# Performance work log

Measured on AMD Instinct MI355X. Metric: run time of the kernel, lower is better.

## Reference

```python
import jax, jax.numpy as jnp
from jax import lax
import numpy as np

B, NW, L, E, H, V = 8192, 4, 16, 128, 128, 64  # batch, words/example, max chars, emsize, hidden, char vocab


def setup_inputs() -> dict:
    key = jax.random.key(0)
    ks = jax.random.split(key, 13)
    s = 0.05
    return {
        "word_ids": jax.random.randint(ks[0], (B, NW, L), 0, V, dtype=jnp.int32),
        "lengths": jax.random.randint(ks[1], (B, NW), 1, L + 1, dtype=jnp.int32),
        "emb_i": jax.random.normal(ks[2], (V, E), jnp.float32),
        "W_ih": jax.random.normal(ks[3], (4 * H, E), jnp.float32) * s,
        "W_hh": jax.random.normal(ks[4], (4 * H, H), jnp.float32) * s,
        "b_ih": jax.random.normal(ks[5], (4 * H,), jnp.float32) * s,
        "b_hh": jax.random.normal(ks[6], (4 * H,), jnp.float32) * s,
        "conv1_w": jax.random.normal(ks[7], (4, 1, 2, 2), jnp.float32) * 0.5,
        "conv1_b": jax.random.normal(ks[8], (4,), jnp.float32) * 0.1,
        "conv2_w": jax.random.normal(ks[9], (8, 4, 2, 2), jnp.float32) * 0.5,
        "conv2_b": jax.random.normal(ks[10], (8,), jnp.float32) * 0.1,
        "scorer_w": jax.random.normal(ks[11], (1, 2 * 2 * 8), jnp.float32) * 0.2,
        "scorer_b": jax.random.normal(ks[12], (1,), jnp.float32) * 0.1,
    }


def reference(word_ids, lengths, emb_i, W_ih, W_hh, b_ih, b_hh,
              conv1_w, conv1_b, conv2_w, conv2_b, scorer_w, scorer_b):
    Bx, NWx, Lx = word_ids.shape
    Hh = W_hh.shape[1]
    BN = Bx * NWx
    # char embeddings for all words, packed: [L, BN, E]
    xs = emb_i[word_ids.reshape(BN, Lx)].transpose(1, 0, 2)
    # ragged lengths -> per-step update mask [L, BN]
    mask = jnp.arange(Lx, dtype=lengths.dtype)[:, None] < lengths.reshape(-1)[None, :]
    h0 = jnp.zeros((BN, Hh), emb_i.dtype)

    def step(carry, xm):
        h, c = carry
        x_t, m = xm
        gates = x_t @ W_ih.T + b_ih + h @ W_hh.T + b_hh  # torch LSTMCell gate order i,f,g,o
        i, f, g, o = jnp.split(gates, 4, axis=-1)
        i = jax.nn.sigmoid(i); f = jax.nn.sigmoid(f)
        g = jnp.tanh(g); o = jax.nn.sigmoid(o)
        c_new = f * c + i * g
        h_new = o * jnp.tanh(c_new)
        m = m[:, None]
        return (jnp.where(m, h_new, h), jnp.where(m, c_new, c)), None

    (h, c), _ = lax.scan(step, (h0, h0), (xs, mask))
    # Model.encode returns the cell state c
    reps = c.reshape(Bx, NWx, Hh)

    # pairwise cosine similarity matrix [B, NW, NW]
    norms = jnp.sqrt(jnp.sum(reps * reps, axis=-1))
    dots = jnp.einsum('bih,bjh->bij', reps, reps)
    cos = dots / (norms[:, :, None] * norms[:, None, :])

    # tiny 2-layer CNN scorer on the NWxNW matrix (NCHW)
    dn = ('NCHW', 'OIHW', 'NCHW')
    x_img = cos[:, None, :, :]
    out = jax.nn.relu(lax.conv_general_dilated(x_img, conv1_w, (1, 1), 'VALID', dimension_numbers=dn)
                      + conv1_b[None, :, None, None])
    out = jax.nn.relu(lax.conv_general_dilated(out, conv2_w, (1, 1), 'VALID', dimension_numbers=dn)
                      + conv2_b[None, :, None, None])
    flat = out.reshape(Bx, -1)  # channel-major flatten matches torch .view
    score = flat @ scorer_w.T + scorer_b
    return jax.nn.sigmoid(score)  # [B, 1] discriminator prob
```

## Files before the change

### kernel.cpp

```cpp
#include <hip/hip_runtime.h>

#define BSZ    8192
#define NWRD   4
#define SEQL   16
#define HDIM   128
#define VOCAB  64
#define NSEQ   (BSZ * NWRD)
#define WGSEQ  32
#define UPB    80
#define BINCAP (UPB * WGSEQ)
#define NUNITS (16 * UPB)

#define AS1 __attribute__((address_space(1)))
#define AS3 __attribute__((address_space(3)))

typedef float    f32x4  __attribute__((ext_vector_type(4)));
typedef float    f32x16 __attribute__((ext_vector_type(16)));
typedef __bf16   bf16x8 __attribute__((ext_vector_type(8)));
typedef _Float16 f16x8  __attribute__((ext_vector_type(8)));
typedef int      i32x4  __attribute__((ext_vector_type(4)));

union AccU { f32x16 v; f32x4 q[4]; float f[16]; };

__device__ __forceinline__ unsigned short f2bf(float f) {
    unsigned int u = __builtin_bit_cast(unsigned int, f);
    return (unsigned short)((u + 0x7fff + ((u >> 16) & 1)) >> 16);
}
__device__ __forceinline__ float sigm(float x) {
    return __builtin_amdgcn_rcpf(1.f + __builtin_amdgcn_exp2f(x * -1.44269504f));
}

__global__ void prep4(const float* __restrict__ emb, const float* __restrict__ W_ih,
                      const float* __restrict__ b_ih, const float* __restrict__ b_hh,
                      const float* __restrict__ W_hh, const int* __restrict__ lengths,
                      unsigned short* __restrict__ P2H, unsigned short* __restrict__ WA,
                      int* __restrict__ perm, int* __restrict__ gh)
{
    __shared__ int lh[16], gbase[16];
    const int blk = blockIdx.x, tid = threadIdx.x;

    if (blk < 128) {
        int idx = blk * 256 + tid;
        int v = idx >> 9, g = (idx >> 7) & 3, j = idx & 127;
        int n = g * 128 + j;
        const f32x4* er = (const f32x4*)(emb  + v * 128);
        const f32x4* wr = (const f32x4*)(W_ih + n * 128);
        f32x4 s4 = er[0] * wr[0];
#pragma unroll
        for (int e = 1; e < 32; ++e) s4 += er[e] * wr[e];
        float s = s4.x + s4.y + s4.z + s4.w + b_ih[n] + b_hh[n];
        int wv = j >> 5, jr = j & 31;
        int d = jr & 3, hl = (jr >> 2) & 1, q = jr >> 3;
        int cc = g * 16 + wv * 4 + hl * 2 + (q >> 1);
        int F  = v * 512 + ((cc ^ (v & 7)) << 3) + (q & 1) * 4 + d;
        P2H[F] = __builtin_bit_cast(unsigned short, (_Float16)s);
    } else if (blk < 384) {
        int idx = (blk - 128) * 256 + tid;
        int jj = idx & 7, lane = (idx >> 3) & 63, kc = (idx >> 9) & 7, tt = idx >> 12;
        int wv = tt >> 2, g = tt & 3;
        int n = g * 128 + wv * 32 + (lane & 31);
        int k = kc * 16 + (lane >> 5) * 8 + jj;
        WA[idx] = f2bf(W_hh[n * 128 + k]);
    } else {
        if (tid < 16) lh[tid] = 0;
        __syncthreads();
        int i = (blk - 384) * 256 + tid;
        int b = 16 - lengths[i];
        int rank = atomicAdd(&lh[b], 1);
        __syncthreads();
        if (tid < 16) gbase[tid] = atomicAdd(&gh[tid], lh[tid]);
        __syncthreads();
        perm[b * BINCAP + gbase[b] + rank] = i;
    }
}

__global__ __launch_bounds__(256, 2) void lstm4(
    const int* __restrict__ word_ids, const int* __restrict__ perm,
    const int* __restrict__ gh, const unsigned short* __restrict__ P2H,
    const unsigned short* __restrict__ WA, float* __restrict__ c_out)
{
    __shared__ __align__(16) unsigned short ptab[VOCAB * 512];
    __shared__ __align__(16) unsigned short hbuf[2][WGSEQ * 128];

    const int tid    = threadIdx.x;
    const int wv     = tid >> 6;
    const int lane   = tid & 63;
    const int lane31 = lane & 31;
    const int hl     = lane >> 5;

    const int u    = blockIdx.x;
    const int b    = u / UPB;
    const int widx = u % UPB;
    const int cnt  = gh[b];
    if (widx * WGSEQ >= cnt) return;
    const int ml   = 16 - b;

    {
        const char* src = (const char*)P2H;
        char*       dst = (char*)ptab;
#pragma unroll
        for (int r = 0; r < 16; ++r) {
            const int off = r * 4096 + wv * 1024;
            __builtin_amdgcn_global_load_lds(
                (const AS1 unsigned int*)(src + off + lane * 16),
                (AS3 unsigned int*)(dst + off), 16, 0, 0);
        }
    }

    bf16x8 afr[4][8];
#pragma unroll
    for (int g = 0; g < 4; ++g)
#pragma unroll
        for (int kc = 0; kc < 8; ++kc)
            afr[g][kc] = *(const bf16x8*)(WA + (((wv * 4 + g) * 8 + kc) * 64 + lane) * 8);

    const int slot = widx * WGSEQ + lane31;
    const int live = slot < cnt;
    const int sid  = live ? perm[b * BINCAP + slot] : 0;
    unsigned long long u0, u1;
    {
        const i32x4* wp = (const i32x4*)(word_ids + sid * SEQL);
        i32x4 a = wp[0], b4 = wp[1], c4 = wp[2], d4 = wp[3];
        unsigned lo0 = (unsigned)(a.x  | (a.y  << 8) | (a.z  << 16) | (a.w  << 24));
        unsigned hi0 = (unsigned)(b4.x | (b4.y << 8) | (b4.z << 16) | (b4.w << 24));
        unsigned lo1 = (unsigned)(c4.x | (c4.y << 8) | (c4.z << 16) | (c4.w << 24));
        unsigned hi1 = (unsigned)(d4.x | (d4.y << 8) | (d4.z << 16) | (d4.w << 24));
        u0 = ((unsigned long long)hi0 << 32) | lo0;
        u1 = ((unsigned long long)hi1 << 32) | lo1;
    }
    __syncthreads();

    f32x4 cq[4] = {{0,0,0,0},{0,0,0,0},{0,0,0,0},{0,0,0,0}};
    const int      rdo_b = lane31 * 256;
    const unsigned xv    = (unsigned)((lane31 & 7) << 4);
    const int      jbase = wv * 32 + 4 * hl;
    const int      ccb   = wv * 4 + hl * 2;

#pragma unroll 1
    for (int t = 0; t < ml; ++t) {
        const int w = (int)(u0 & 63);
        u0 = (u0 >> 8) | (u1 << 56); u1 >>= 8;

        AccU acc[4];
        {
            const char*    rowp = (const char*)ptab + (w << 10);
            const unsigned wx   = (unsigned)((w & 7) << 4);
#pragma unroll
            for (int g = 0; g < 4; ++g)
#pragma unroll
                for (int s = 0; s < 2; ++s) {
                    const unsigned off = ((unsigned)((g * 16 + ccb + s) << 4)) ^ wx;
                    f16x8 hv = *(const f16x8*)(rowp + off);
#pragma unroll
                    for (int k = 0; k < 8; ++k)
                        acc[g].f[s * 8 + k] = (float)hv[k];
                }
        }

        if (t > 0) {
            const char* hr = (const char*)hbuf[t & 1];
            bf16x8 bfv[8];
#pragma unroll
            for (int kc = 0; kc < 8; ++kc)
                bfv[kc] = *(const bf16x8*)(hr + rdo_b +
                              (((unsigned)(kc * 32 + hl * 16)) ^ xv));
#pragma unroll
            for (int kc = 0; kc < 8; ++kc) {
                const bf16x8 bb = bfv[kc];
#pragma unroll
                for (int g = 0; g < 4; ++g)
                    acc[g].v = __builtin_amdgcn_mfma_f32_32x32x16_bf16(
                        afr[g][kc], bb, acc[g].v, 0, 0, 0);
            }
        }

        const int wr = (t < ml - 1);
        char* hw = (char*)hbuf[(t + 1) & 1];
#pragma unroll
        for (int q = 0; q < 4; ++q) {
            float hv4[4];
#pragma unroll
            for (int d = 0; d < 4; ++d) {
                const int r = q * 4 + d;
                float ei = __builtin_amdgcn_exp2f(acc[0].f[r] * -1.44269504f);
                float ef = __builtin_amdgcn_exp2f(acc[1].f[r] * -1.44269504f);
                float eg = __builtin_amdgcn_exp2f(acc[2].f[r] *  2.88539008f);
                float fg  = __builtin_amdgcn_rcpf(1.f + ef);
                float igg = (eg - 1.f) *
                            __builtin_amdgcn_rcpf((1.f + ei) * (1.f + eg));
                float cn = cq[q][d] * fg + igg;
                cq[q][d] = cn;
                if (wr) {
                    float eo = __builtin_amdgcn_exp2f(acc[3].f[r] * -1.44269504f);
                    float ec = __builtin_amdgcn_exp2f(cn * 2.88539008f);
                    hv4[d] = (ec - 1.f) *
                             __builtin_amdgcn_rcpf((1.f + eo) * (1.f + ec));
                }
            }
            if (wr) {
                unsigned int plo_, phi_;
                asm("v_cvt_pk_bf16_f32 %0, %1, %2"
                    : "=v"(plo_) : "v"(hv4[0]), "v"(hv4[1]));
                asm("v_cvt_pk_bf16_f32 %0, %1, %2"
                    : "=v"(phi_) : "v"(hv4[2]), "v"(hv4[3]));
                unsigned long long pu_ =
                    ((unsigned long long)phi_ << 32) | plo_;
                *(unsigned long long*)(hw + rdo_b +
                    (((unsigned)(wv * 64 + q * 16)) ^ xv) + hl * 8) = pu_;
            }
        }
        if (wr) __syncthreads();
    }

    if (live) {
#pragma unroll
        for (int q = 0; q < 4; ++q)
            *(f32x4*)(c_out + sid * HDIM + jbase + 8 * q) = cq[q];
    }
}

__global__ __launch_bounds__(256) void epilogue(
    const float* __restrict__ c_ws,
    const float* __restrict__ conv1_w, const float* __restrict__ conv1_b,
    const float* __restrict__ conv2_w, const float* __restrict__ conv2_b,
    const float* __restrict__ scorer_w, const float* __restrict__ scorer_b,
    float* __restrict__ out)
{
    __shared__ __align__(16) float reps[8 * NWRD * HDIM];
    __shared__ float gram_s[8 * 16];

    const int tid = threadIdx.x;
    const int b0  = blockIdx.x * 8;

    for (int i = tid; i < 8 * NWRD * HDIM; i += 256)
        reps[i] = c_ws[b0 * NWRD * HDIM + i];
    __syncthreads();

    const int bt  = tid >> 5;
    const int sub = tid & 31;

    float dval = 0.f;
    if (sub < 16) {
        int i = sub >> 2, j = sub & 3;
        const f32x4* ci = (const f32x4*)(reps + (bt * 4 + i) * HDIM);
        const f32x4* cj = (const f32x4*)(reps + (bt * 4 + j) * HDIM);
        f32x4 s4 = {0.f, 0.f, 0.f, 0.f};
        for (int k = 0; k < HDIM / 4; ++k) s4 += ci[k] * cj[k];
        dval = s4.x + s4.y + s4.z + s4.w;
        gram_s[bt * 16 + sub] = dval;
    }
    __syncthreads();
    float cosv = 0.f;
    if (sub < 16) {
        int i = sub >> 2, j = sub & 3;
        float di = gram_s[bt * 16 + i * 4 + i];
        float dj = gram_s[bt * 16 + j * 4 + j];
        cosv = __fdividef(dval, sqrtf(di * dj));
    }
    __syncthreads();
    if (sub < 16) gram_s[bt * 16 + sub] = cosv;
    __syncthreads();

    if (sub == 0) {
        float img[4][4];
#pragma unroll
        for (int i = 0; i < 4; ++i)
#pragma unroll
            for (int j = 0; j < 4; ++j) img[i][j] = gram_s[bt * 16 + i * 4 + j];

        float o1[4][3][3];
#pragma unroll
        for (int ch = 0; ch < 4; ++ch) {
            float w00 = conv1_w[ch*4+0], w01 = conv1_w[ch*4+1];
            float w10 = conv1_w[ch*4+2], w11 = conv1_w[ch*4+3];
            float bb  = conv1_b[ch];
#pragma unroll
            for (int y = 0; y < 3; ++y)
#pragma unroll
                for (int x = 0; x < 3; ++x) {
                    float s = bb + w00*img[y][x]   + w01*img[y][x+1]
                                 + w10*img[y+1][x] + w11*img[y+1][x+1];
                    o1[ch][y][x] = s > 0.f ? s : 0.f;
                }
        }
        float sc = scorer_b[0];
#pragma unroll
        for (int oc = 0; oc < 8; ++oc) {
            float bb = conv2_b[oc];
#pragma unroll
            for (int y = 0; y < 2; ++y)
#pragma unroll
                for (int x = 0; x < 2; ++x) {
                    float s = bb;
#pragma unroll
                    for (int ic = 0; ic < 4; ++ic) {
                        const float* w = conv2_w + oc * 16 + ic * 4;
                        s += w[0]*o1[ic][y][x]   + w[1]*o1[ic][y][x+1]
                           + w[2]*o1[ic][y+1][x] + w[3]*o1[ic][y+1][x+1];
                    }
                    float rl = s > 0.f ? s : 0.f;
                    sc += rl * scorer_w[oc * 4 + y * 2 + x];
                }
        }
        out[blockIdx.x * 8 + bt] = sigm(sc);
    }
}

extern "C" void kernel_launch(void* const* d_in, const int* in_sizes, int n_in,
                              void* d_out, int out_size, void* d_ws, size_t ws_size,
                              hipStream_t stream)
{
    const int*   word_ids = (const int*)d_in[0];
    const int*   lengths  = (const int*)d_in[1];
    const float* emb      = (const float*)d_in[2];
    const float* W_ih     = (const float*)d_in[3];
    const float* W_hh     = (const float*)d_in[4];
    const float* b_ih     = (const float*)d_in[5];
    const float* b_hh     = (const float*)d_in[6];
    const float* conv1_w  = (const float*)d_in[7];
    const float* conv1_b  = (const float*)d_in[8];
    const float* conv2_w  = (const float*)d_in[9];
    const float* conv2_b  = (const float*)d_in[10];
    const float* scorer_w = (const float*)d_in[11];
    const float* scorer_b = (const float*)d_in[12];
    float* out = (float*)d_out;

    char* ws = (char*)d_ws;
    unsigned short* P2H  = (unsigned short*)(ws + 0);
    unsigned short* WA   = (unsigned short*)(ws + (128<<10));
    int*            perm = (int*)(ws + (256<<10));
    int*            gh   = (int*)(ws + (416<<10));
    float*          c_ws = (float*)(ws + (512<<10));

    hipMemsetAsync(gh, 0, 16 * sizeof(int), stream);
    prep4   <<<512,   256, 0, stream>>>(emb, W_ih, b_ih, b_hh, W_hh, lengths,
                                        P2H, WA, perm, gh);
    lstm4   <<<NUNITS, 256, 0, stream>>>(word_ids, perm, gh, P2H, WA, c_ws);
    epilogue<<<BSZ / 8, 256, 0, stream>>>(c_ws, conv1_w, conv1_b, conv2_w, conv2_b,
                                          scorer_w, scorer_b, out);
}
```

Baseline: 172.3 us.

## Load input projections via identity MFMA and offload exp to FMA polynomial

The precomputed input-projection table is now loaded as f16 vectors and added into the accumulators with two identity-matrix f16 MFMAs per gate, instead of per-element f16-to-f32 conversions. The table layout in the prep kernel changes to match. Two of the transcendental exp2 calls per element are replaced by a polynomial exp2 built from FMAs, and the gate math is refactored to use a single reciprocal instead of two. The aim is to move work off the transcendental and VALU conversion paths onto the matrix and FMA units. The cost is extra MFMA instructions and a polynomial with no overflow handling.

```diff
diff --git a/kernel.cpp b/kernel.cpp
--- a/kernel.cpp
+++ b/kernel.cpp
@@ -29,6 +29,18 @@
 __device__ __forceinline__ float sigm(float x) {
     return __builtin_amdgcn_rcpf(1.f + __builtin_amdgcn_exp2f(x * -1.44269504f));
 }
+__device__ __forceinline__ float pexp2(float y) {
+    float n = __builtin_rintf(y);
+    float f = y - n;
+    float p = 1.3333558e-3f;
+    p = __builtin_fmaf(p, f, 9.6181291e-3f);
+    p = __builtin_fmaf(p, f, 5.5504109e-2f);
+    p = __builtin_fmaf(p, f, 2.4022651e-1f);
+    p = __builtin_fmaf(p, f, 6.9314718e-1f);
+    p = __builtin_fmaf(p, f, 1.0f);
+    int e = (int)n;
+    return __builtin_bit_cast(float, __builtin_bit_cast(int, p) + (e << 23));
+}
 
 __global__ void prep4(const float* __restrict__ emb, const float* __restrict__ W_ih,
                       const float* __restrict__ b_ih, const float* __restrict__ b_hh,
@@ -49,10 +61,8 @@
 #pragma unroll
         for (int e = 1; e < 32; ++e) s4 += er[e] * wr[e];
         float s = s4.x + s4.y + s4.z + s4.w + b_ih[n] + b_hh[n];
-        int wv = j >> 5, jr = j & 31;
-        int d = jr & 3, hl = (jr >> 2) & 1, q = jr >> 3;
-        int cc = g * 16 + wv * 4 + hl * 2 + (q >> 1);
-        int F  = v * 512 + ((cc ^ (v & 7)) << 3) + (q & 1) * 4 + d;
+        int cj = g * 16 + (j >> 3);
+        int F  = v * 512 + ((cj ^ (v & 7)) << 3) + (j & 7);
         P2H[F] = __builtin_bit_cast(unsigned short, (_Float16)s);
     } else if (blk < 384) {
         int idx = (blk - 128) * 256 + tid;
@@ -114,6 +124,14 @@
         for (int kc = 0; kc < 8; ++kc)
             afr[g][kc] = *(const bf16x8*)(WA + (((wv * 4 + g) * 8 + kc) * 64 + lane) * 8);
 
+    f16x8 idA0, idA1;
+#pragma unroll
+    for (int jj = 0; jj < 8; ++jj) {
+        idA0[jj] = (_Float16)((lane31 == hl * 8 + jj)      ? 1.f : 0.f);
+        idA1[jj] = (_Float16)((lane31 == 16 + hl * 8 + jj) ? 1.f : 0.f);
+    }
+    const f32x16 ZED = {0,0,0,0, 0,0,0,0, 0,0,0,0, 0,0,0,0};
+
     const int slot = widx * WGSEQ + lane31;
     const int live = slot < cnt;
     const int sid  = live ? perm[b * BINCAP + slot] : 0;
@@ -134,29 +152,25 @@
     const int      rdo_b = lane31 * 256;
     const unsigned xv    = (unsigned)((lane31 & 7) << 4);
     const int      jbase = wv * 32 + 4 * hl;
-    const int      ccb   = wv * 4 + hl * 2;
 
 #pragma unroll 1
     for (int t = 0; t < ml; ++t) {
         const int w = (int)(u0 & 63);
         u0 = (u0 >> 8) | (u1 << 56); u1 >>= 8;
+        const unsigned rowb = ((unsigned)w << 10);
+        const unsigned wx   = (unsigned)((w & 7) << 4);
+
+        f16x8 pf[4][2];
+#pragma unroll
+        for (int g = 0; g < 4; ++g)
+#pragma unroll
+            for (int s = 0; s < 2; ++s) {
+                const unsigned cj =
+                    ((unsigned)((g * 16 + wv * 4 + s * 2 + hl) << 4)) ^ wx;
+                pf[g][s] = *(const f16x8*)((const char*)ptab + rowb + cj);
+            }
 
         AccU acc[4];
-        {
-            const char*    rowp = (const char*)ptab + (w << 10);
-            const unsigned wx   = (unsigned)((w & 7) << 4);
-#pragma unroll
-            for (int g = 0; g < 4; ++g)
-#pragma unroll
-                for (int s = 0; s < 2; ++s) {
-                    const unsigned off = ((unsigned)((g * 16 + ccb + s) << 4)) ^ wx;
-                    f16x8 hv = *(const f16x8*)(rowp + off);
-#pragma unroll
-                    for (int k = 0; k < 8; ++k)
-                        acc[g].f[s * 8 + k] = (float)hv[k];
-                }
-        }
-
         if (t > 0) {
             const char* hr = (const char*)hbuf[t & 1];
             bf16x8 bfv[8];
@@ -165,12 +179,23 @@
                 bfv[kc] = *(const bf16x8*)(hr + rdo_b +
                               (((unsigned)(kc * 32 + hl * 16)) ^ xv));
 #pragma unroll
-            for (int kc = 0; kc < 8; ++kc) {
-                const bf16x8 bb = bfv[kc];
-#pragma unroll
-                for (int g = 0; g < 4; ++g)
+            for (int g = 0; g < 4; ++g) {
+                acc[g].v = __builtin_amdgcn_mfma_f32_32x32x16_f16(
+                    idA0, pf[g][0], ZED, 0, 0, 0);
+                acc[g].v = __builtin_amdgcn_mfma_f32_32x32x16_f16(
+                    idA1, pf[g][1], acc[g].v, 0, 0, 0);
+#pragma unroll
+                for (int kc = 0; kc < 8; ++kc)
                     acc[g].v = __builtin_amdgcn_mfma_f32_32x32x16_bf16(
-                        afr[g][kc], bb, acc[g].v, 0, 0, 0);
+                        afr[g][kc], bfv[kc], acc[g].v, 0, 0, 0);
+            }
+        } else {
+#pragma unroll
+            for (int g = 0; g < 4; ++g) {
+                acc[g].v = __builtin_amdgcn_mfma_f32_32x32x16_f16(
+                    idA0, pf[g][0], ZED, 0, 0, 0);
+                acc[g].v = __builtin_amdgcn_mfma_f32_32x32x16_f16(
+                    idA1, pf[g][1], acc[g].v, 0, 0, 0);
             }
         }
 
@@ -184,15 +209,15 @@
                 const int r = q * 4 + d;
                 float ei = __builtin_amdgcn_exp2f(acc[0].f[r] * -1.44269504f);
                 float ef = __builtin_amdgcn_exp2f(acc[1].f[r] * -1.44269504f);
-                float eg = __builtin_amdgcn_exp2f(acc[2].f[r] *  2.88539008f);
-                float fg  = __builtin_amdgcn_rcpf(1.f + ef);
-                float igg = (eg - 1.f) *
-                            __builtin_amdgcn_rcpf((1.f + ei) * (1.f + eg));
-                float cn = cq[q][d] * fg + igg;
+                float eg = pexp2(acc[2].f[r] * 2.88539008f);
+                float ai = 1.f + ei, af = 1.f + ef, ag = 1.f + eg;
+                float t1 = ai * ag;
+                float R  = __builtin_amdgcn_rcpf(t1 * af);
+                float cn = __builtin_fmaf(cq[q][d], t1, (eg - 1.f) * af) * R;
                 cq[q][d] = cn;
                 if (wr) {
                     float eo = __builtin_amdgcn_exp2f(acc[3].f[r] * -1.44269504f);
-                    float ec = __builtin_amdgcn_exp2f(cn * 2.88539008f);
+                    float ec = pexp2(cn * 2.88539008f);
                     hv4[d] = (ec - 1.f) *
                              __builtin_amdgcn_rcpf((1.f + eo) * (1.f + ec));
                 }
```

Result: slower. 192.0 us (+11.4%).

## Use persistent LSTM blocks with atomic work-queue over length bins

Applied to the files above, without the earlier changes.

Replaces the fixed grid of 1280 blocks, where most exit early, with 512 persistent blocks. Each block takes 32-sequence work items from a global atomic counter, handing out the longest bins first. The block therefore loads the embedding-projection table and W_hh fragments once and reuses them across many items, which amortises setup and balances load. The gate math is also changed to use one reciprocal for the cell update. The cost is an atomic and a barrier per work item.

```diff
diff --git a/kernel.cpp b/kernel.cpp
--- a/kernel.cpp
+++ b/kernel.cpp
@@ -9,7 +9,7 @@
 #define WGSEQ  32
 #define UPB    80
 #define BINCAP (UPB * WGSEQ)
-#define NUNITS (16 * UPB)
+#define NBLK   512
 
 #define AS1 __attribute__((address_space(1)))
 #define AS3 __attribute__((address_space(3)))
@@ -76,11 +76,12 @@
 
 __global__ __launch_bounds__(256, 2) void lstm4(
     const int* __restrict__ word_ids, const int* __restrict__ perm,
-    const int* __restrict__ gh, const unsigned short* __restrict__ P2H,
+    int* __restrict__ gh, const unsigned short* __restrict__ P2H,
     const unsigned short* __restrict__ WA, float* __restrict__ c_out)
 {
     __shared__ __align__(16) unsigned short ptab[VOCAB * 512];
     __shared__ __align__(16) unsigned short hbuf[2][WGSEQ * 128];
+    __shared__ int tick_s;
 
     const int tid    = threadIdx.x;
     const int wv     = tid >> 6;
@@ -88,13 +89,6 @@
     const int lane31 = lane & 31;
     const int hl     = lane >> 5;
 
-    const int u    = blockIdx.x;
-    const int b    = u / UPB;
-    const int widx = u % UPB;
-    const int cnt  = gh[b];
-    if (widx * WGSEQ >= cnt) return;
-    const int ml   = 16 - b;
-
     {
         const char* src = (const char*)P2H;
         char*       dst = (char*)ptab;
@@ -114,108 +108,136 @@
         for (int kc = 0; kc < 8; ++kc)
             afr[g][kc] = *(const bf16x8*)(WA + (((wv * 4 + g) * 8 + kc) * 64 + lane) * 8);
 
-    const int slot = widx * WGSEQ + lane31;
-    const int live = slot < cnt;
-    const int sid  = live ? perm[b * BINCAP + slot] : 0;
-    unsigned long long u0, u1;
-    {
-        const i32x4* wp = (const i32x4*)(word_ids + sid * SEQL);
-        i32x4 a = wp[0], b4 = wp[1], c4 = wp[2], d4 = wp[3];
-        unsigned lo0 = (unsigned)(a.x  | (a.y  << 8) | (a.z  << 16) | (a.w  << 24));
-        unsigned hi0 = (unsigned)(b4.x | (b4.y << 8) | (b4.z << 16) | (b4.w << 24));
-        unsigned lo1 = (unsigned)(c4.x | (c4.y << 8) | (c4.z << 16) | (c4.w << 24));
-        unsigned hi1 = (unsigned)(d4.x | (d4.y << 8) | (d4.z << 16) | (d4.w << 24));
-        u0 = ((unsigned long long)hi0 << 32) | lo0;
-        u1 = ((unsigned long long)hi1 << 32) | lo1;
-    }
-    __syncthreads();
-
-    f32x4 cq[4] = {{0,0,0,0},{0,0,0,0},{0,0,0,0},{0,0,0,0}};
+    int ghs[16];
+#pragma unroll
+    for (int i = 0; i < 16; ++i) ghs[i] = gh[i];
+    int tot = 0;
+#pragma unroll
+    for (int i = 0; i < 16; ++i) tot += (ghs[i] + 31) >> 5;
+
     const int      rdo_b = lane31 * 256;
     const unsigned xv    = (unsigned)((lane31 & 7) << 4);
     const int      jbase = wv * 32 + 4 * hl;
     const int      ccb   = wv * 4 + hl * 2;
 
+    for (;;) {
+        if (tid == 0) tick_s = atomicAdd(gh + 16, 1);
+        __syncthreads();
+        const int k = tick_s;
+        if (k >= tot) break;
+
+        int rem = k, bsel = 0, found = 0;
+#pragma unroll
+        for (int b2 = 0; b2 < 16; ++b2) {
+            int nb = (ghs[b2] + 31) >> 5;
+            if (!found) {
+                if (rem < nb) { bsel = b2; found = 1; }
+                else rem -= nb;
+            }
+        }
+        const int widx = rem;
+        const int cnt  = ghs[bsel];
+        const int ml   = 16 - bsel;
+
+        const int slot = widx * WGSEQ + lane31;
+        const int live = slot < cnt;
+        const int sid  = live ? perm[bsel * BINCAP + slot] : 0;
+        unsigned long long u0, u1;
+        {
+            const i32x4* wp = (const i32x4*)(word_ids + sid * SEQL);
+            i32x4 a = wp[0], b4 = wp[1], c4 = wp[2], d4 = wp[3];
+            unsigned lo0 = (unsigned)(a.x  | (a.y  << 8) | (a.z  << 16) | (a.w  << 24));
+            unsigned hi0 = (unsigned)(b4.x | (b4.y << 8) | (b4.z << 16) | (b4.w << 24));
+            unsigned lo1 = (unsigned)(c4.x | (c4.y << 8) | (c4.z << 16) | (c4.w << 24));
+            unsigned hi1 = (unsigned)(d4.x | (d4.y << 8) | (d4.z << 16) | (d4.w << 24));
+            u0 = ((unsigned long long)hi0 << 32) | lo0;
+            u1 = ((unsigned long long)hi1 << 32) | lo1;
+        }
+
+        f32x4 cq[4] = {{0,0,0,0},{0,0,0,0},{0,0,0,0},{0,0,0,0}};
+
 #pragma unroll 1
-    for (int t = 0; t < ml; ++t) {
-        const int w = (int)(u0 & 63);
-        u0 = (u0 >> 8) | (u1 << 56); u1 >>= 8;
-
-        AccU acc[4];
-        {
-            const char*    rowp = (const char*)ptab + (w << 10);
-            const unsigned wx   = (unsigned)((w & 7) << 4);
-#pragma unroll
-            for (int g = 0; g < 4; ++g)
-#pragma unroll
-                for (int s = 0; s < 2; ++s) {
-                    const unsigned off = ((unsigned)((g * 16 + ccb + s) << 4)) ^ wx;
-                    f16x8 hv = *(const f16x8*)(rowp + off);
-#pragma unroll
-                    for (int k = 0; k < 8; ++k)
-                        acc[g].f[s * 8 + k] = (float)hv[k];
-                }
-        }
-
-        if (t > 0) {
-            const char* hr = (const char*)hbuf[t & 1];
-            bf16x8 bfv[8];
-#pragma unroll
-            for (int kc = 0; kc < 8; ++kc)
-                bfv[kc] = *(const bf16x8*)(hr + rdo_b +
-                              (((unsigned)(kc * 32 + hl * 16)) ^ xv));
-#pragma unroll
-            for (int kc = 0; kc < 8; ++kc) {
-                const bf16x8 bb = bfv[kc];
+        for (int t = 0; t < ml; ++t) {
+            const int w = (int)(u0 & 63);
+            u0 = (u0 >> 8) | (u1 << 56); u1 >>= 8;
+
+            AccU acc[4];
+            {
+                const char*    rowp = (const char*)ptab + (w << 10);
+                const unsigned wx   = (unsigned)((w & 7) << 4);
 #pragma unroll
                 for (int g = 0; g < 4; ++g)
-                    acc[g].v = __builtin_amdgcn_mfma_f32_32x32x16_bf16(
-                        afr[g][kc], bb, acc[g].v, 0, 0, 0);
+#pragma unroll
+                    for (int s = 0; s < 2; ++s) {
+                        const unsigned off =
+                            ((unsigned)((g * 16 + ccb + s) << 4)) ^ wx;
+                        f16x8 hv = *(const f16x8*)(rowp + off);
+#pragma unroll
+                        for (int kk = 0; kk < 8; ++kk)
+                            acc[g].f[s * 8 + kk] = (float)hv[kk];
+                    }
             }
-        }
-
-        const int wr = (t < ml - 1);
-        char* hw = (char*)hbuf[(t + 1) & 1];
-#pragma unroll
-        for (int q = 0; q < 4; ++q) {
-            float hv4[4];
-#pragma unroll
-            for (int d = 0; d < 4; ++d) {
-                const int r = q * 4 + d;
-                float ei = __builtin_amdgcn_exp2f(acc[0].f[r] * -1.44269504f);
-                float ef = __builtin_amdgcn_exp2f(acc[1].f[r] * -1.44269504f);
-                float eg = __builtin_amdgcn_exp2f(acc[2].f[r] *  2.88539008f);
-                float fg  = __builtin_amdgcn_rcpf(1.f + ef);
-                float igg = (eg - 1.f) *
-                            __builtin_amdgcn_rcpf((1.f + ei) * (1.f + eg));
-                float cn = cq[q][d] * fg + igg;
-                cq[q][d] = cn;
+
+            if (t > 0) {
+                const char* hr = (const char*)hbuf[t & 1];
+                bf16x8 bfv[8];
+#pragma unroll
+                for (int kc = 0; kc < 8; ++kc)
+                    bfv[kc] = *(const bf16x8*)(hr + rdo_b +
+                                  (((unsigned)(kc * 32 + hl * 16)) ^ xv));
+#pragma unroll
+                for (int kc = 0; kc < 8; ++kc) {
+                    const bf16x8 bb = bfv[kc];
+#pragma unroll
+                    for (int g = 0; g < 4; ++g)
+                        acc[g].v = __builtin_amdgcn_mfma_f32_32x32x16_bf16(
+                            afr[g][kc], bb, acc[g].v, 0, 0, 0);
+                }
+            }
+
+            const int wr = (t < ml - 1);
+            char* hw = (char*)hbuf[(t + 1) & 1];
+#pragma unroll
+            for (int q = 0; q < 4; ++q) {
+                float hv4[4];
+#pragma unroll
+                for (int d = 0; d < 4; ++d) {
+                    const int r = q * 4 + d;
+                    float ei = __builtin_amdgcn_exp2f(acc[0].f[r] * -1.44269504f);
+                    float ef = __builtin_amdgcn_exp2f(acc[1].f[r] * -1.44269504f);
+                    float eg = __builtin_amdgcn_exp2f(acc[2].f[r] *  2.88539008f);
+                    float ai = 1.f + ei, af = 1.f + ef, ag = 1.f + eg;
+                    float t1 = ai * ag;
+                    float R  = __builtin_amdgcn_rcpf(t1 * af);
+                    float cn = __builtin_fmaf(cq[q][d], t1, (eg - 1.f) * af) * R;
+                    cq[q][d] = cn;
+                    if (wr) {
+                        float eo = __builtin_amdgcn_exp2f(acc[3].f[r] * -1.44269504f);
+                        float ec = __builtin_amdgcn_exp2f(cn * 2.88539008f);
+                        hv4[d] = (ec - 1.f) *
+                                 __builtin_amdgcn_rcpf((1.f + eo) * (1.f + ec));
+                    }
+                }
                 if (wr) {
-                    float eo = __builtin_amdgcn_exp2f(acc[3].f[r] * -1.44269504f);
-                    float ec = __builtin_amdgcn_exp2f(cn * 2.88539008f);
-                    hv4[d] = (ec - 1.f) *
-                             __builtin_amdgcn_rcpf((1.f + eo) * (1.f + ec));
+                    unsigned int plo_, phi_;
+                    asm("v_cvt_pk_bf16_f32 %0, %1, %2"
+                        : "=v"(plo_) : "v"(hv4[0]), "v"(hv4[1]));
+                    asm("v_cvt_pk_bf16_f32 %0, %1, %2"
+                        : "=v"(phi_) : "v"(hv4[2]), "v"(hv4[3]));
+                    unsigned long long pu_ =
+                        ((unsigned long long)phi_ << 32) | plo_;
+                    *(unsigned long long*)(hw + rdo_b +
+                        (((unsigned)(wv * 64 + q * 16)) ^ xv) + hl * 8) = pu_;
                 }
             }
-            if (wr) {
-                unsigned int plo_, phi_;
-                asm("v_cvt_pk_bf16_f32 %0, %1, %2"
-                    : "=v"(plo_) : "v"(hv4[0]), "v"(hv4[1]));
-                asm("v_cvt_pk_bf16_f32 %0, %1, %2"
-                    : "=v"(phi_) : "v"(hv4[2]), "v"(hv4[3]));
-                unsigned long long pu_ =
-                    ((unsigned long long)phi_ << 32) | plo_;
-                *(unsigned long long*)(hw + rdo_b +
-                    (((unsigned)(wv * 64 + q * 16)) ^ xv) + hl * 8) = pu_;
-            }
-        }
-        if (wr) __syncthreads();
-    }
-
-    if (live) {
-#pragma unroll
-        for (int q = 0; q < 4; ++q)
-            *(f32x4*)(c_out + sid * HDIM + jbase + 8 * q) = cq[q];
+            if (wr) __syncthreads();
+        }
+
+        if (live) {
+#pragma unroll
+            for (int q = 0; q < 4; ++q)
+                *(f32x4*)(c_out + sid * HDIM + jbase + 8 * q) = cq[q];
+        }
     }
 }
 
@@ -332,10 +354,10 @@
     int*            gh   = (int*)(ws + (416<<10));
     float*          c_ws = (float*)(ws + (512<<10));
 
-    hipMemsetAsync(gh, 0, 16 * sizeof(int), stream);
-    prep4   <<<512,   256, 0, stream>>>(emb, W_ih, b_ih, b_hh, W_hh, lengths,
-                                        P2H, WA, perm, gh);
-    lstm4   <<<NUNITS, 256, 0, stream>>>(word_ids, perm, gh, P2H, WA, c_ws);
+    hipMemsetAsync(gh, 0, 17 * sizeof(int), stream);
+    prep4   <<<512,  256, 0, stream>>>(emb, W_ih, b_ih, b_hh, W_hh, lengths,
+                                       P2H, WA, perm, gh);
+    lstm4   <<<NBLK, 256, 0, stream>>>(word_ids, perm, gh, P2H, WA, c_ws);
     epilogue<<<BSZ / 8, 256, 0, stream>>>(c_ws, conv1_w, conv1_b, conv2_w, conv2_b,
                                           scorer_w, scorer_b, out);
 }
```

Result: slower. 202.2 us (+17.3%).
